# Optimization experiments

Measured on AMD Instinct MI355X. Metric: run time of the kernel, lower is better.

The kernel has to match this reference:

```python
import jax, jax.numpy as jnp
import numpy as np

B = 16384          # batch (positions)
F = 32             # active features per perspective per sample
INPUT_SIZE = 40960
HIDDEN_SIZE = 256
L2_SIZE = 32


def _embedding_bag_sum(weight, indices, offsets, num_bags):
    """torch.nn.EmbeddingBag(mode='sum') with offsets."""
    n = indices.shape[0]
    # segment id of each flat index: which bag it belongs to
    seg = jnp.searchsorted(offsets, jnp.arange(n), side='right') - 1
    return jax.ops.segment_sum(weight[indices], seg, num_segments=num_bags)


def setup_inputs() -> dict:
    key = jax.random.key(0)
    ks = jax.random.split(key, 6)
    white_indices = jax.random.randint(ks[0], (B * F,), 0, INPUT_SIZE)
    black_indices = jax.random.randint(ks[1], (B * F,), 0, INPUT_SIZE)
    offsets = jnp.arange(B, dtype=jnp.int64 if jax.config.jax_enable_x64 else jnp.int32) * F
    stm = jax.random.bernoulli(ks[2], 0.5, (B,))
    ft_weight = jax.random.uniform(ks[3], (INPUT_SIZE, HIDDEN_SIZE), minval=-0.05, maxval=0.05)
    ft_bias = jnp.zeros((HIDDEN_SIZE,), jnp.float32)
    # kaiming_normal (fan_in mode) approximations
    l1_w = jax.random.normal(ks[4], (L2_SIZE, 2 * HIDDEN_SIZE)) * np.float32(np.sqrt(2.0 / (2 * HIDDEN_SIZE)))
    l1_b = jnp.zeros((L2_SIZE,), jnp.float32)
    l2_w = jax.random.normal(ks[5], (1, L2_SIZE)) * np.float32(np.sqrt(1.0 / L2_SIZE))
    l2_b = jnp.zeros((1,), jnp.float32)
    return {
        'white_indices': white_indices, 'white_offsets': offsets,
        'black_indices': black_indices, 'black_offsets': offsets,
        'stm': stm,
        'ft_weight': ft_weight, 'ft_bias': ft_bias,
        'l1_w': l1_w, 'l1_b': l1_b, 'l2_w': l2_w, 'l2_b': l2_b,
    }


def reference(white_indices, white_offsets, black_indices, black_offsets, stm,
              ft_weight, ft_bias, l1_w, l1_b, l2_w, l2_b):
    nb = white_offsets.shape[0]
    white_acc = _embedding_bag_sum(ft_weight, white_indices, white_offsets, nb) + ft_bias
    black_acc = _embedding_bag_sum(ft_weight, black_indices, black_offsets, nb) + ft_bias
    white_acc = jnp.clip(white_acc, 0.0, 1.0)
    black_acc = jnp.clip(black_acc, 0.0, 1.0)
    stm_col = stm[:, None]
    us = jnp.where(stm_col, black_acc, white_acc)
    them = jnp.where(stm_col, white_acc, black_acc)
    combined = jnp.concatenate([us, them], axis=1)          # [B, 2H]
    hidden = jnp.clip(combined @ l1_w.T + l1_b, 0.0, 1.0)   # [B, L2]
    return hidden @ l2_w.T + l2_b                            # [B, 1]
```

## Files before the change

kernel.cpp:

```cpp
#include <hip/hip_runtime.h>
#include <hip/hip_fp16.h>


typedef _Float16 h2 __attribute__((ext_vector_type(2)));
typedef float    fx4 __attribute__((ext_vector_type(4)));
typedef unsigned ux4 __attribute__((ext_vector_type(4)));

#define QSCALE 2048.0f
#define QINV   (1.0f / 2048.0f)
#define TBL_BYTES  (40960ull * 256ull)
#define FEAT_BYTES (16384ull * 512ull * 2ull)
#define CHUNK_UX4  (40960 * 4)

__device__ __forceinline__ float clamp01(float x) { return fminf(fmaxf(x, 0.0f), 1.0f); }

__device__ __forceinline__ float fdot2f(h2 a, h2 b, float c) {
#if __has_builtin(__builtin_amdgcn_fdot2)
    return __builtin_amdgcn_fdot2(a, b, c, false);
#else
    return c + (float)a.x * (float)b.x + (float)a.y * (float)b.y;
#endif
}
__device__ __forceinline__ unsigned pk2(float lo, float hi) {
    h2 v; v.x = (_Float16)lo; v.y = (_Float16)hi;
    return __builtin_bit_cast(unsigned, v);
}
__device__ __forceinline__ h2 as_h2(unsigned u) { return __builtin_bit_cast(h2, u); }
__device__ __forceinline__ unsigned short f16b(float x) {
    return __builtin_bit_cast(unsigned short, (_Float16)x);
}

__device__ __forceinline__ void acc4(unsigned d, int& a0, int& a1, int& a2, int& a3) {
#if __has_builtin(__builtin_amdgcn_sdot4)
    a0 = __builtin_amdgcn_sdot4((int)d, 0x00000001, a0, false);
    a1 = __builtin_amdgcn_sdot4((int)d, 0x00000100, a1, false);
    a2 = __builtin_amdgcn_sdot4((int)d, 0x00010000, a2, false);
    a3 = __builtin_amdgcn_sdot4((int)d, 0x01000000, a3, false);
#else
    a0 += (int)(signed char)(d);
    a1 += (int)(signed char)(d >> 8);
    a2 += (int)(signed char)(d >> 16);
    a3 += (int)(signed char)(d >> 24);
#endif
}

__device__ __forceinline__ unsigned pkb(fx4 v) {
    const int q0 = __float2int_rn(v.x * QSCALE) & 255;
    const int q1 = __float2int_rn(v.y * QSCALE) & 255;
    const int q2 = __float2int_rn(v.z * QSCALE) & 255;
    const int q3 = __float2int_rn(v.w * QSCALE) & 255;
    return (unsigned)(q0 | (q1 << 8) | (q2 << 16) | (q3 << 24));
}
template <int SPLIT>
__global__ __launch_bounds__(256)
void cvt_f32_i8(const fx4* __restrict__ src, ux4* __restrict__ dst, int n16) {
    const int i = blockIdx.x * 256 + threadIdx.x;
    if (i >= n16) return;
    const fx4 a = __builtin_nontemporal_load(&src[4 * i]);
    const fx4 b = __builtin_nontemporal_load(&src[4 * i + 1]);
    const fx4 c = __builtin_nontemporal_load(&src[4 * i + 2]);
    const fx4 d = __builtin_nontemporal_load(&src[4 * i + 3]);
    ux4 o; o.x = pkb(a); o.y = pkb(b); o.z = pkb(c); o.w = pkb(d);
    if (SPLIT) {
        const int row   = i >> 4;
        const int sub   = i & 3;
        const int chunk = (i >> 2) & 3;
        dst[chunk * CHUNK_UX4 + row * 4 + sub] = o;
    } else {
        dst[i] = o;
    }
}

#define FOLDA(T, arr, NK, M)                                         \
    _Pragma("unroll")                                                \
    for (int k_ = 0; k_ < (NK) / 2; ++k_) {                          \
        const T fa_ = arr[k_], fb_ = arr[k_ + (NK) / 2];             \
        const T send_ = (lane & (M)) ? fa_ : fb_;                    \
        const T recv_ = __shfl_xor(send_, (M), 64);                  \
        arr[k_] = ((lane & (M)) ? fb_ : fa_) + recv_;                \
    }

__global__ __launch_bounds__(256, 8)
void nnue_gather(const int* __restrict__ wi, const int* __restrict__ bi,
                 const void* __restrict__ stmv,
                 const ux4* __restrict__ tbl,
                 const float* __restrict__ ftbf,
                 unsigned short* __restrict__ feat)
{
    const int tid  = threadIdx.x;
    const int lane = tid & 63;
    const int g     = blockIdx.x;
    const int chunk = g & 3;
    const int half  = (g >> 2) & 1;
    const int grp   = g >> 3;

    const unsigned sprobe = __builtin_nontemporal_load(&((const unsigned*)stmv)[lane]);
    const unsigned long long isf32 = __ballot(sprobe == 0x3f800000u);
    const unsigned long long isbig = __ballot(sprobe > 1u);
    const int smode = isf32 ? 2 : (isbig ? 1 : 0);

    const int q  = lane & 15;
    const int rs = lane >> 4;

    const int colq = 4 * q + 2 * ((lane >> 4) & 1) + (lane >> 5);
    const int colg = chunk * 64 + colq;
    const float bias = ftbf[colg];

    const unsigned* __restrict__ tcU =
        (const unsigned*)(tbl + chunk * CHUNK_UX4);

    const int b0base = half * 8192 + grp * 32 + (tid >> 6) * 8;
    const int* __restrict__ ip = (lane < 32) ? wi : bi;

    int vidx = __builtin_nontemporal_load(&ip[(b0base << 5) + (lane & 31)]);

    for (int bb = 0; bb < 8; ++bb) {
        const int b = b0base + bb;
        int vnext = 0;
        if (bb < 7)
            vnext = __builtin_nontemporal_load(&ip[((b + 1) << 5) + (lane & 31)]);

        unsigned wdw[8], bdw[8];
#pragma unroll
        for (int k = 0; k < 8; ++k) {
            const int iw = __shfl(vidx, rs + 4 * k, 64);
            wdw[k] = tcU[iw * 16 + q];
        }
#pragma unroll
        for (int k = 0; k < 8; ++k) {
            const int ib = __shfl(vidx, 32 + rs + 4 * k, 64);
            bdw[k] = tcU[ib * 16 + q];
        }

        int wa[4] = {0, 0, 0, 0}, ba[4] = {0, 0, 0, 0};
#pragma unroll
        for (int k = 0; k < 8; ++k) acc4(wdw[k], wa[0], wa[1], wa[2], wa[3]);
#pragma unroll
        for (int k = 0; k < 8; ++k) acc4(bdw[k], ba[0], ba[1], ba[2], ba[3]);

        FOLDA(int, wa, 4, 16)  FOLDA(int, ba, 4, 16)
        FOLDA(int, wa, 2, 32)  FOLDA(int, ba, 2, 32)

        const float W  = clamp01((float)wa[0] * QINV + bias);
        const float Bk = clamp01((float)ba[0] * QINV + bias);

        int s;
        if (smode == 0)      s = __builtin_nontemporal_load(&((const int*)stmv)[b]);
        else if (smode == 1) s = __builtin_nontemporal_load(&((const unsigned char*)stmv)[b]);
        else                 s = (__builtin_nontemporal_load(&((const float*)stmv)[b]) != 0.0f);

        const float us = s ? Bk : W;
        const float th = s ? W : Bk;
        feat[b * 512 + colg]       = f16b(us);
        feat[b * 512 + 256 + colg] = f16b(th);

        vidx = vnext;
    }
}

__global__ __launch_bounds__(256, 4)
void nnue_mlp(const ux4* __restrict__ feat4,
              const float4* __restrict__ l1w,
              const float* __restrict__ l1b,
              const float* __restrict__ l2w,
              const float* __restrict__ l2b,
              float* __restrict__ out)
{
    __shared__ uint2 pkA[64 * 32];
    __shared__ uint2 pkB[64 * 32];
    __shared__ float lbS[32];
    __shared__ float lwS[32];
    __shared__ float l2bS;

    const int tid  = threadIdx.x;
    const int lane = tid & 63;
    const int lm   = lane & 31;

    {
        const int kg = tid >> 6;
#pragma unroll
        for (int i = 0; i < 8; ++i) {
            const int k = kg * 8 + i;
            const float4 a = l1w[k * 128 + 2 * lane];
            const float4 c = l1w[k * 128 + 2 * lane + 1];
            const int sw = lane * 32 + (k ^ lm);
            pkA[sw] = make_uint2(pk2(a.x, a.y), pk2(a.z, a.w));
            pkB[sw] = make_uint2(pk2(c.x, c.y), pk2(c.z, c.w));
        }
        if (tid < 32) { lbS[tid] = l1b[tid]; lwS[tid] = l2w[tid]; }
        if (tid == 0) l2bS = l2b[0];
    }
    __syncthreads();

    const int b = blockIdx.x * 4 + (tid >> 6);

    const ux4 f = feat4[b * 64 + lane];
    const h2 f0 = as_h2(f.x), f1 = as_h2(f.y), f2 = as_h2(f.z), f3 = as_h2(f.w);

    const uint2* __restrict__ pa = pkA + lane * 32;
    const uint2* __restrict__ pb = pkB + lane * 32;

    float hid[32];
#pragma unroll
    for (int k = 0; k < 32; ++k) {
        const uint2 wa = pa[k ^ lm];
        const uint2 wb = pb[k ^ lm];
        float s = fdot2f(as_h2(wa.x), f0, 0.0f);
        s = fdot2f(as_h2(wa.y), f1, s);
        s = fdot2f(as_h2(wb.x), f2, s);
        hid[k] = fdot2f(as_h2(wb.y), f3, s);
    }

    FOLDA(float, hid, 32, 32)
    FOLDA(float, hid, 16, 16)
    FOLDA(float, hid, 8, 8)
    FOLDA(float, hid, 4, 4)
    FOLDA(float, hid, 2, 2)
    const float S = hid[0] + __shfl_xor(hid[0], 1, 64);
    const int kk = (lane >> 1) & 31;

    float v = clamp01(S + lbS[kk]) * lwS[kk];
#pragma unroll
    for (int m = 2; m <= 32; m <<= 1) v += __shfl_xor(v, m, 64);

    if (lane == 0) out[b] = v + l2bS;
}

template <int TBL>
__global__ __launch_bounds__(256, 4)
void nnue_fused(const int* __restrict__ wi, const int* __restrict__ bi,
                const void* __restrict__ stmv, const void* __restrict__ tblv,
                const float4* __restrict__ ftb, const float4* __restrict__ l1w,
                const float* __restrict__ l1b, const float* __restrict__ l2w,
                const float* __restrict__ l2b, float* __restrict__ out)
{
    __shared__ uint2 pk_us[64 * 32];
    __shared__ uint2 pk_th[64 * 32];
    __shared__ float lbS[32];
    __shared__ float lwS[32];
    __shared__ float l2bS;

    const int tid  = threadIdx.x;
    const int lane = tid & 63;
    const int lm   = lane & 31;
    {
        const int kg = tid >> 6;
#pragma unroll
        for (int i = 0; i < 8; ++i) {
            const int k  = kg * 8 + i;
            const float4 u = l1w[k * 128 + lane];
            const float4 t = l1w[k * 128 + 64 + lane];
            const int sw = lane * 32 + (k ^ lm);
            pk_us[sw] = make_uint2(pk2(u.x, u.y), pk2(u.z, u.w));
            pk_th[sw] = make_uint2(pk2(t.x, t.y), pk2(t.z, t.w));
        }
        if (tid < 32) { lbS[tid] = l1b[tid]; lwS[tid] = l2w[tid]; }
        if (tid == 0) l2bS = l2b[0];
    }
    __syncthreads();

    const unsigned sprobe = ((const unsigned*)stmv)[lane];
    const unsigned long long isf32 = __ballot(sprobe == 0x3f800000u);
    const unsigned long long isbig = __ballot(sprobe > 1u);
    const int smode = isf32 ? 2 : (isbig ? 1 : 0);

    const int gw = blockIdx.x * 4 + (tid >> 6);
    const int q  = lane >> 2;
    const int r  = lane & 3;
    const float4 bvv = ftb[lane];
    const uint2* __restrict__ pu = pk_us + lane * 32;
    const uint2* __restrict__ pt = pk_th + lane * 32;

    for (int bb = 0; bb < 4; ++bb) {
        const int b = gw * 4 + bb;
        const int vidx = ((lane < 32) ? wi : bi)[(b << 5) + lm];
        float aw0, aw1, aw2, aw3, ab0, ab1, ab2, ab3;

        if (TBL == 1) {
            const uint4* __restrict__ t4 = (const uint4*)tblv;
            int iw[8], ib[8];
#pragma unroll
            for (int jj = 0; jj < 8; ++jj) {
                iw[jj] = __shfl(vidx, 4 * jj + r, 64);
                ib[jj] = __shfl(vidx, 32 + 4 * jj + r, 64);
            }
            int wa[16], ba[16];
#pragma unroll
            for (int i = 0; i < 16; ++i) { wa[i] = 0; ba[i] = 0; }
#pragma unroll
            for (int jj = 0; jj < 8; ++jj) {
                const uint4 rw = t4[iw[jj] * 16 + q];
                acc4(rw.x, wa[0], wa[1], wa[2], wa[3]);
                acc4(rw.y, wa[4], wa[5], wa[6], wa[7]);
                acc4(rw.z, wa[8], wa[9], wa[10], wa[11]);
                acc4(rw.w, wa[12], wa[13], wa[14], wa[15]);
            }
#pragma unroll
            for (int jj = 0; jj < 8; ++jj) {
                const uint4 rb = t4[ib[jj] * 16 + q];
                acc4(rb.x, ba[0], ba[1], ba[2], ba[3]);
                acc4(rb.y, ba[4], ba[5], ba[6], ba[7]);
                acc4(rb.z, ba[8], ba[9], ba[10], ba[11]);
                acc4(rb.w, ba[12], ba[13], ba[14], ba[15]);
            }
#pragma unroll
            for (int i = 0; i < 16; ++i) {
                wa[i] += __shfl_xor(wa[i], 1, 64);
                ba[i] += __shfl_xor(ba[i], 1, 64);
            }
#pragma unroll
            for (int i = 0; i < 16; ++i) {
                wa[i] += __shfl_xor(wa[i], 2, 64);
                ba[i] += __shfl_xor(ba[i], 2, 64);
            }
            int ws_[4], bs[4];
#pragma unroll
            for (int j = 0; j < 4; ++j) {
                const int wlo = (lane & 1) ? wa[4 + j]  : wa[j];
                const int whi = (lane & 1) ? wa[12 + j] : wa[8 + j];
                ws_[j] = (lane & 2) ? whi : wlo;
                const int blo = (lane & 1) ? ba[4 + j]  : ba[j];
                const int bhi = (lane & 1) ? ba[12 + j] : ba[8 + j];
                bs[j] = (lane & 2) ? bhi : blo;
            }
            aw0 = (float)ws_[0] * QINV; aw1 = (float)ws_[1] * QINV;
            aw2 = (float)ws_[2] * QINV; aw3 = (float)ws_[3] * QINV;
            ab0 = (float)bs[0] * QINV;  ab1 = (float)bs[1] * QINV;
            ab2 = (float)bs[2] * QINV;  ab3 = (float)bs[3] * QINV;
        } else {
            const float4* __restrict__ tbl = (const float4*)tblv;
            aw0 = aw1 = aw2 = aw3 = 0.f;
            ab0 = ab1 = ab2 = ab3 = 0.f;
#pragma unroll 8
            for (int j = 0; j < 32; ++j) {
                const int iw  = __builtin_amdgcn_readlane(vidx, j);
                const int ibk = __builtin_amdgcn_readlane(vidx, j + 32);
                const float4 rw = tbl[iw * 64 + lane];
                const float4 rb = tbl[ibk * 64 + lane];
                aw0 += rw.x; aw1 += rw.y; aw2 += rw.z; aw3 += rw.w;
                ab0 += rb.x; ab1 += rb.y; ab2 += rb.z; ab3 += rb.w;
            }
        }

        aw0 = clamp01(aw0 + bvv.x); aw1 = clamp01(aw1 + bvv.y);
        aw2 = clamp01(aw2 + bvv.z); aw3 = clamp01(aw3 + bvv.w);
        ab0 = clamp01(ab0 + bvv.x); ab1 = clamp01(ab1 + bvv.y);
        ab2 = clamp01(ab2 + bvv.z); ab3 = clamp01(ab3 + bvv.w);

        int s;
        if (smode == 0)      s = ((const int*)stmv)[b];
        else if (smode == 1) s = ((const unsigned char*)stmv)[b];
        else                 s = (((const float*)stmv)[b] != 0.0f);

        const float u0 = s ? ab0 : aw0, u1 = s ? ab1 : aw1;
        const float u2 = s ? ab2 : aw2, u3 = s ? ab3 : aw3;
        const float t0 = s ? aw0 : ab0, t1 = s ? aw1 : ab1;
        const float t2 = s ? aw2 : ab2, t3 = s ? aw3 : ab3;

        h2 u01; u01.x = (_Float16)u0; u01.y = (_Float16)u1;
        h2 u23; u23.x = (_Float16)u2; u23.y = (_Float16)u3;
        h2 t01; t01.x = (_Float16)t0; t01.y = (_Float16)t1;
        h2 t23; t23.x = (_Float16)t2; t23.y = (_Float16)t3;

        float hid[32];
#pragma unroll
        for (int k = 0; k < 32; ++k) {
            const uint2 wu = pu[k ^ lm];
            const uint2 wt = pt[k ^ lm];
            float sacc = fdot2f(as_h2(wu.x), u01, 0.0f);
            sacc = fdot2f(as_h2(wu.y), u23, sacc);
            sacc = fdot2f(as_h2(wt.x), t01, sacc);
            hid[k] = fdot2f(as_h2(wt.y), t23, sacc);
        }

        FOLDA(float, hid, 32, 32)
        FOLDA(float, hid, 16, 16)
        FOLDA(float, hid, 8, 8)
        FOLDA(float, hid, 4, 4)
        FOLDA(float, hid, 2, 2)
        const float S = hid[0] + __shfl_xor(hid[0], 1, 64);
        const int kk = (lane >> 1) & 31;

        float v = clamp01(S + lbS[kk]) * lwS[kk];
#pragma unroll
        for (int m = 2; m <= 32; m <<= 1) v += __shfl_xor(v, m, 64);

        if (lane == 0) out[b] = v + l2bS;
    }
}

extern "C" void kernel_launch(void* const* d_in, const int* in_sizes, int n_in,
                              void* d_out, int out_size, void* d_ws, size_t ws_size,
                              hipStream_t stream) {
    const int*    wi  = (const int*)d_in[0];
    const int*    bi  = (const int*)d_in[2];
    const void*   stm = d_in[4];
    const float*  ftw = (const float*)d_in[5];
    const float*  ftbf = (const float*)d_in[6];
    const float4* l1w = (const float4*)d_in[7];
    const float*  l1b = (const float*)d_in[8];
    const float*  l2w = (const float*)d_in[9];
    const float*  l2b = (const float*)d_in[10];
    float* out = (float*)d_out;

    const int n16 = (40960 * 256) / 16;

    if (ws_size >= TBL_BYTES + FEAT_BYTES) {
        unsigned short* feat = (unsigned short*)((char*)d_ws + TBL_BYTES);
        hipLaunchKernelGGL((cvt_f32_i8<1>), dim3(n16 / 256), dim3(256), 0, stream,
                           (const fx4*)ftw, (ux4*)d_ws, n16);
        hipLaunchKernelGGL(nnue_gather, dim3(2048), dim3(256), 0, stream,
                           wi, bi, stm, (const ux4*)d_ws, ftbf, feat);
        hipLaunchKernelGGL(nnue_mlp, dim3(4096), dim3(256), 0, stream,
                           (const ux4*)feat, l1w, l1b, l2w, l2b, out);
    } else if (ws_size >= TBL_BYTES) {
        hipLaunchKernelGGL((cvt_f32_i8<0>), dim3(n16 / 256), dim3(256), 0, stream,
                           (const fx4*)ftw, (ux4*)d_ws, n16);
        hipLaunchKernelGGL((nnue_fused<1>), dim3(1024), dim3(256), 0, stream,
                           wi, bi, stm, (const void*)d_ws, (const float4*)ftbf,
                           l1w, l1b, l2w, l2b, out);
    } else {
        hipLaunchKernelGGL((nnue_fused<0>), dim3(1024), dim3(256), 0, stream,
                           wi, bi, stm, (const void*)ftw, (const float4*)ftbf,
                           l1w, l1b, l2w, l2b, out);
    }
}
```

Baseline: 167.5 us.

## Double-buffer embedding gather loads across batch iterations in gather kernel

The gather kernel now prefetches all eight index rows up front and software-pipelines the table loads, issuing the next sample's 16 row loads into a second register buffer before accumulating the current one. Launch bounds drop from 8 to 4 waves per SIMD so the extra live registers fit. This trades occupancy for more memory-level parallelism within each wave, aiming to hide gather latency in the bandwidth-bound lookup phase.

```diff
diff --git a/kernel.cpp b/kernel.cpp
--- a/kernel.cpp
+++ b/kernel.cpp
@@ -80,7 +80,7 @@
         arr[k_] = ((lane & (M)) ? fb_ : fa_) + recv_;                \
     }
 
-__global__ __launch_bounds__(256, 8)
+__global__ __launch_bounds__(256, 4)
 void nnue_gather(const int* __restrict__ wi, const int* __restrict__ bi,
                  const void* __restrict__ stmv,
                  const ux4* __restrict__ tbl,
@@ -112,31 +112,42 @@
     const int b0base = half * 8192 + grp * 32 + (tid >> 6) * 8;
     const int* __restrict__ ip = (lane < 32) ? wi : bi;
 
-    int vidx = __builtin_nontemporal_load(&ip[(b0base << 5) + (lane & 31)]);
-
+    int vq[8];
+#pragma unroll
+    for (int k = 0; k < 8; ++k)
+        vq[k] = __builtin_nontemporal_load(&ip[((b0base + k) << 5) + (lane & 31)]);
+
+    unsigned wdw[2][8], bdw[2][8];
+
+#define ISSUE_LOADS(BB, P)                                           \
+    _Pragma("unroll")                                                \
+    for (int k_ = 0; k_ < 8; ++k_) {                                 \
+        const int iw_ = __shfl(vq[BB], rs + 4 * k_, 64);             \
+        wdw[P][k_] = tcU[iw_ * 16 + q];                              \
+    }                                                                \
+    _Pragma("unroll")                                                \
+    for (int k_ = 0; k_ < 8; ++k_) {                                 \
+        const int ib_ = __shfl(vq[BB], 32 + rs + 4 * k_, 64);        \
+        bdw[P][k_] = tcU[ib_ * 16 + q];                              \
+    }
+
+    ISSUE_LOADS(0, 0)
+
+#pragma unroll
     for (int bb = 0; bb < 8; ++bb) {
+        const int P = bb & 1;
+        if (bb < 7) {
+            if ((bb & 1) == 0) { ISSUE_LOADS(bb + 1, 1) }
+            else               { ISSUE_LOADS(bb + 1, 0) }
+        }
+
         const int b = b0base + bb;
-        int vnext = 0;
-        if (bb < 7)
-            vnext = __builtin_nontemporal_load(&ip[((b + 1) << 5) + (lane & 31)]);
-
-        unsigned wdw[8], bdw[8];
-#pragma unroll
-        for (int k = 0; k < 8; ++k) {
-            const int iw = __shfl(vidx, rs + 4 * k, 64);
-            wdw[k] = tcU[iw * 16 + q];
-        }
-#pragma unroll
-        for (int k = 0; k < 8; ++k) {
-            const int ib = __shfl(vidx, 32 + rs + 4 * k, 64);
-            bdw[k] = tcU[ib * 16 + q];
-        }
 
         int wa[4] = {0, 0, 0, 0}, ba[4] = {0, 0, 0, 0};
 #pragma unroll
-        for (int k = 0; k < 8; ++k) acc4(wdw[k], wa[0], wa[1], wa[2], wa[3]);
-#pragma unroll
-        for (int k = 0; k < 8; ++k) acc4(bdw[k], ba[0], ba[1], ba[2], ba[3]);
+        for (int k = 0; k < 8; ++k) acc4(wdw[P][k], wa[0], wa[1], wa[2], wa[3]);
+#pragma unroll
+        for (int k = 0; k < 8; ++k) acc4(bdw[P][k], ba[0], ba[1], ba[2], ba[3]);
 
         FOLDA(int, wa, 4, 16)  FOLDA(int, ba, 4, 16)
         FOLDA(int, wa, 2, 32)  FOLDA(int, ba, 2, 32)
@@ -153,9 +164,8 @@
         const float th = s ? W : Bk;
         feat[b * 512 + colg]       = f16b(us);
         feat[b * 512 + 256 + colg] = f16b(th);
-
-        vidx = vnext;
-    }
+    }
+#undef ISSUE_LOADS
 }
 
 __global__ __launch_bounds__(256, 4)
```

Measured after the change: 162.2 us. 1.03x faster.
